# Performance work log

Measured on AMD Instinct MI355X. Metric: run time of the kernel, lower is better.

Reference implementation:

```python
import jax, jax.numpy as jnp
import numpy as np

REPEAT = 3
N, M, APM = 8192, 256, 32   # atoms, molecules, atoms per molecule
F_IN, D = 16, 64            # input atom features, hidden dim (d_e=d_v=d_u)


def _build_graph():
    k1 = np.arange(APM - 1)
    k2 = np.arange(APM - 2)
    pairs = np.concatenate([np.stack([k1, k1 + 1], 1), np.stack([k2, k2 + 2], 1)], 0)  # (61,2)
    base = (np.arange(M) * APM)[:, None, None]
    all_pairs = (pairs[None] + base).reshape(-1, 2)  # (E,2), upper triangular (left<right)
    return all_pairs[:, 0].astype(np.int32), all_pairs[:, 1].astype(np.int32)


def setup_inputs() -> dict:
    key = jax.random.key(0)
    ks = jax.random.split(key, 10)
    left, right = _build_graph()
    E = left.shape[0]  # 15616
    rng = np.random.default_rng(0)
    orders = rng.integers(1, 3, size=E).astype(np.float32)  # bond orders in {1,2}
    adj = np.zeros((N, N), np.float32)
    adj[left, right] = orders
    atom_in_mol = np.zeros((N, M), bool)
    atom_in_mol[np.arange(N), np.arange(N) // APM] = True
    bond_mol = left // APM
    bond_in_mol = np.zeros((E, M), bool)
    bond_in_mol[np.arange(E), bond_mol] = True

    def dense(k, fan_in, fan_out):
        return jax.random.normal(k, (fan_in, fan_out), jnp.float32) / np.sqrt(fan_in)

    return {
        'atoms': jax.random.normal(ks[0], (N, F_IN), jnp.float32),
        'adjacency_map': jnp.asarray(adj),
        'left_idxs': jnp.asarray(left),
        'right_idxs': jnp.asarray(right),
        'atom_in_mol': jnp.asarray(atom_in_mol),
        'bond_in_mol': jnp.asarray(bond_in_mol),
        'W_fe': dense(ks[1], 1, D), 'b_fe': jnp.zeros((D,), jnp.float32),
        'W_fv': dense(ks[2], F_IN, D), 'b_fv': jnp.zeros((D,), jnp.float32),
        'W_fu': dense(ks[3], F_IN, D), 'b_fu': jnp.zeros((D,), jnp.float32),
        'W_pe': dense(ks[4], 4 * D + 1, D), 'b_pe': jnp.zeros((D,), jnp.float32),
        'W_pv': dense(ks[5], 4 * D, D), 'b_pv': jnp.zeros((D,), jnp.float32),
        'W_pu': dense(ks[6], 4 * D, D), 'b_pu': jnp.zeros((D,), jnp.float32),
    }


def _graphnet(atoms, adjacency_map, left_idxs, right_idxs, atom_in_mol, bond_in_mol,
              W_fe, b_fe, W_fv, b_fv, W_fu, b_fu, W_pe, b_pe, W_pv, b_pv, W_pu, b_pu):
    n_atoms = atoms.shape[0]
    n_mols = atom_in_mol.shape[1]
    atom_mol = jnp.argmax(atom_in_mol, axis=1)   # (N,)  one mol per atom
    bond_mol = jnp.argmax(bond_in_mol, axis=1)   # (E,)  one mol per bond

    # f_e / f_v / f_u : initial edge, node, global embeddings
    bond_orders = adjacency_map[left_idxs, right_idxs]                  # (E,)
    h_e = jnp.tanh(bond_orders[:, None] @ W_fe + b_fe)                  # (E,D)
    h_v = jnp.tanh(atoms @ W_fv + b_fv)                                 # (N,D)
    atoms_per_mol = jax.ops.segment_sum(atoms, atom_mol, num_segments=n_mols)
    h_u = jnp.tanh(atoms_per_mol @ W_fu + b_fu)                         # (M,D)
    h_e0, h_v0, h_u0 = h_e, h_v, h_u

    for _ in range(REPEAT):
        # phi_e: per-edge update. TF's global term reduces over the feature
        # axis with keepdims -> a scalar per bond (faithful reproduction).
        h_left = h_v[left_idxs]
        h_right = h_v[right_idxs]
        u_e = jnp.sum(h_u[bond_mol], axis=1, keepdims=True)             # (E,1)
        h_e = jnp.tanh(jnp.concatenate([h_e, h_e0, h_left, h_right, u_e], -1) @ W_pe + b_pe)

        # rho_e_v: masked sum of edge features per incident atom == scatter-add
        h_e_bar_i = (jnp.zeros((n_atoms, h_e.shape[1]), h_e.dtype)
                     .at[left_idxs].add(h_e).at[right_idxs].add(h_e))   # (N,D)
        u_v = h_u[atom_mol]                                             # (N,D)
        h_v = jnp.tanh(jnp.concatenate([h_v, h_v0, h_e_bar_i, u_v], -1) @ W_pv + b_pv)

        # rho_e_u / rho_v_u: masked sums per molecule == segment sums
        h_e_bar = jax.ops.segment_sum(h_e, bond_mol, num_segments=n_mols)
        h_v_bar = jax.ops.segment_sum(h_v, atom_mol, num_segments=n_mols)
        h_u = jnp.tanh(jnp.concatenate([h_u, h_u0, h_e_bar, h_v_bar], -1) @ W_pu + b_pu)

    # default f_r = lambda *x: x[0] -> final edge representations
    return h_e


def reference(atoms, adjacency_map, left_idxs, right_idxs, atom_in_mol, bond_in_mol,
              W_fe, b_fe, W_fv, b_fv, W_fu, b_fu, W_pe, b_pe, W_pv, b_pv, W_pu, b_pu):
    return _graphnet(atoms, adjacency_map, left_idxs, right_idxs, atom_in_mol, bond_in_mol,
                     W_fe, b_fe, W_fv, b_fv, W_fu, b_fu, W_pe, b_pe, W_pv, b_pv, W_pu, b_pu)
```

## Files before the change

kernel.cpp:

```cpp
#include <hip/hip_runtime.h>

#define NATOMS 8192
#define NMOLS  256
#define APM    32
#define EPM    61
#define D      64
#define FIN    16
#define SE     72

typedef __bf16 bf16x8 __attribute__((ext_vector_type(8)));
typedef float  f32x4  __attribute__((ext_vector_type(4)));

#define MFMA_BF16(a, b, c) __builtin_amdgcn_mfma_f32_16x16x32_bf16((a), (b), (c), 0, 0, 0)

__device__ __forceinline__ ushort f2bf(float x) {
    uint u = __float_as_uint(x);
    u += 0x7fffu + ((u >> 16) & 1u);
    return (ushort)(u >> 16);
}
__device__ __forceinline__ float bf2f(ushort h) {
    return __uint_as_float(((uint)h) << 16);
}
__device__ __forceinline__ void split2(float x, ushort& h, ushort& l) {
    ushort hh = f2bf(x);
    h = hh;
    l = f2bf(x - bf2f(hh));
}
__device__ __forceinline__ float fast_tanh(float x) {
    float e = __builtin_amdgcn_exp2f(x * 2.885390081777926f);
    float r = __builtin_amdgcn_rcpf(e + 1.0f);
    return __builtin_fmaf(-2.0f, r, 1.0f);
}

union FragU { ushort u[8]; bf16x8 v; };

__device__ __forceinline__ void mfma3s(const ushort* pH, const ushort* pL, int o,
                                       bf16x8 wH, bf16x8 wL,
                                       f32x4& H, f32x4& La, f32x4& Lb) {
    bf16x8 ah = *(const bf16x8*)(pH + o);
    bf16x8 al = *(const bf16x8*)(pL + o);
    H  = MFMA_BF16(ah, wH, H);
    La = MFMA_BF16(al, wH, La);
    Lb = MFMA_BF16(ah, wL, Lb);
}

__global__ __launch_bounds__(512, 2) void graphnet_kernel(
    const float* __restrict__ atoms,
    const float* __restrict__ adj,
    const int*   __restrict__ left,
    const int*   __restrict__ right,
    const float* __restrict__ Wfe, const float* __restrict__ bfe,
    const float* __restrict__ Wfv, const float* __restrict__ bfv,
    const float* __restrict__ Wfu, const float* __restrict__ bfu,
    const float* __restrict__ Wpe, const float* __restrict__ bpe,
    const float* __restrict__ Wpv, const float* __restrict__ bpv,
    const float* __restrict__ Wpu, const float* __restrict__ bpu,
    float* __restrict__ out)
{
    __shared__ __align__(16) ushort heH[2][64 * SE], heL[2][64 * SE];
    __shared__ __align__(16) ushort hvH[2][APM * SE], hvL[2][APM * SE];
    __shared__ __align__(16) ushort huH[D], huL[D];
    __shared__ float huF[D], hu0F[D];
    __shared__ float atoms_s[APM * FIN];
    __shared__ float apm_s[FIN];
    __shared__ float bo_s[EPM];
    __shared__ float parte[4][D];
    __shared__ float part2[2][D];
    __shared__ float hebar[D];
    __shared__ float phiu_part[8][D];
    __shared__ int   lloc[EPM], rloc[EPM];
    __shared__ int   inc[APM][4];

    const int tid  = threadIdx.x;
    const int lane = tid & 63;
    const int w    = tid >> 6;
    const int nt   = w & 3;
    const int mt2  = w >> 2;
    const int cb   = __builtin_amdgcn_readfirstlane(nt) * 16;
    const int lr   = lane & 15;
    const int kb   = lane >> 4;
    const int m    = blockIdx.x;

    if (tid < EPM) {
        int gl = left [m * EPM + tid];
        int gr = right[m * EPM + tid];
        lloc[tid] = gl - m * APM;
        rloc[tid] = gr - m * APM;
        bo_s[tid] = adj[(size_t)gl * NATOMS + gr];
    }
    if (tid < APM * FIN) atoms_s[tid] = atoms[(size_t)m * (APM * FIN) + tid];

    FragU feH[8], feL[8], fvH[8], fvL[8];
    #pragma unroll
    for (int s = 0; s < 8; ++s) {
        if (s == 2 || s == 3) continue;
        #pragma unroll
        for (int j = 0; j < 8; ++j) {
            split2(Wpe[(s * 32 + kb * 8 + j) * D + cb + lr], feH[s].u[j], feL[s].u[j]);
            split2(Wpv[(s * 32 + kb * 8 + j) * D + cb + lr], fvH[s].u[j], fvL[s].u[j]);
        }
    }
    float wpu_reg[32];
    #pragma unroll
    for (int kk = 0; kk < 32; ++kk)
        wpu_reg[kk] = Wpu[(w * 32 + kk) * D + lane];
    const float bias_e = bpe[cb + lr];
    const float w5_e   = Wpe[4 * D * D + cb + lr];
    const float bias_v = bpv[cb + lr];
    const float bpu_l  = bpu[lane];

    __syncthreads();

    if (tid < APM) {
        int dg = 0;
        for (int e = 0; e < EPM; ++e) {
            if (lloc[e] == tid) inc[tid][dg++] = e;
            if (rloc[e] == tid) inc[tid][dg++] = e;
        }
        for (int j = dg; j < 4; ++j) inc[tid][j] = 63;
    }
    if (tid < FIN) {
        float s = 0.f;
        for (int a = 0; a < APM; ++a) s += atoms_s[a * FIN + tid];
        apm_s[tid] = s;
    }
    #pragma unroll
    for (int i = 0; i < 4; ++i) {
        int idx = tid + 512 * i;
        int a = idx >> 6, c = idx & 63;
        float acc = bfv[c];
        #pragma unroll
        for (int f = 0; f < FIN; ++f) acc += atoms_s[a * FIN + f] * Wfv[f * D + c];
        float t = fast_tanh(acc);
        ushort h, l; split2(t, h, l);
        hvH[0][a * SE + c] = h; hvL[0][a * SE + c] = l;
    }
    #pragma unroll
    for (int i = 0; i < 8; ++i) {
        int idx = tid + 512 * i;
        int e = idx >> 6, c = idx & 63;
        float t = 0.f;
        if (e < EPM) t = fast_tanh(bo_s[e] * Wfe[c] + bfe[c]);
        ushort h, l; split2(t, h, l);
        heH[0][e * SE + c] = h; heL[0][e * SE + c] = l;
        if (e >= EPM) { heH[1][e * SE + c] = 0; heL[1][e * SE + c] = 0; }
    }
    __syncthreads();

    float hu_val;
    {
        float acc = bfu[lane];
        #pragma unroll
        for (int f = 0; f < FIN; ++f) acc += apm_s[f] * Wfu[f * D + lane];
        hu_val = fast_tanh(acc);
        if (w == 7) {
            huF[lane] = hu_val; hu0F[lane] = hu_val;
            split2(hu_val, huH[lane], huL[lane]);
        }
    }

    const int col  = cb + lr;
    const int e0   = mt2 * 16 + lr;
    const int e1   = e0 + 32;
    const int ec1  = (e1 < EPM) ? e1 : EPM - 1;
    const int la0  = lloc[e0],  ra0 = rloc[e0];
    const int la1  = lloc[ec1], ra1 = rloc[ec1];
    const int ofk  = kb * 8;
    const int arow = mt2 * 16 + lr;
    const int ie0 = inc[arow][0], ie1 = inc[arow][1];
    const int ie2 = inc[arow][2], ie3 = inc[arow][3];

    f32x4 cE0 = {bias_e, bias_e, bias_e, bias_e};
    f32x4 cE1 = cE0;
    f32x4 cV  = {bias_v, bias_v, bias_v, bias_v};
    {
        FragU w2h, w2l, w3h, w3l, v2h, v2l, v3h, v3l;
        #pragma unroll
        for (int j = 0; j < 8; ++j) {
            split2(Wpe[(2 * 32 + kb * 8 + j) * D + cb + lr], w2h.u[j], w2l.u[j]);
            split2(Wpe[(3 * 32 + kb * 8 + j) * D + cb + lr], w3h.u[j], w3l.u[j]);
            split2(Wpv[(2 * 32 + kb * 8 + j) * D + cb + lr], v2h.u[j], v2l.u[j]);
            split2(Wpv[(3 * 32 + kb * 8 + j) * D + cb + lr], v3h.u[j], v3l.u[j]);
        }
        f32x4 z0 = {0,0,0,0}, z1 = {0,0,0,0}, z2 = {0,0,0,0},
              z3 = {0,0,0,0}, z4 = {0,0,0,0}, z5 = {0,0,0,0};
        mfma3s(heH[0] + e0*SE,  heL[0] + e0*SE,  ofk,      w2h.v, w2l.v, cE0, z0, z1);
        mfma3s(heH[0] + e1*SE,  heL[0] + e1*SE,  ofk,      w2h.v, w2l.v, cE1, z2, z3);
        mfma3s(heH[0] + e0*SE,  heL[0] + e0*SE,  32 + ofk, w3h.v, w3l.v, cE0, z0, z1);
        mfma3s(heH[0] + e1*SE,  heL[0] + e1*SE,  32 + ofk, w3h.v, w3l.v, cE1, z2, z3);
        mfma3s(hvH[0] + arow*SE, hvL[0] + arow*SE, ofk,      v2h.v, v2l.v, cV, z4, z5);
        mfma3s(hvH[0] + arow*SE, hvL[0] + arow*SE, 32 + ofk, v3h.v, v3l.v, cV, z4, z5);
        cE0 += z0 + z1; cE1 += z2 + z3; cV += z4 + z5;
    }

    int cur = 0;
    for (int it = 0; it < 3; ++it) {
        const ushort* heHc = heH[cur]; const ushort* heLc = heL[cur];
        const ushort* hvHc = hvH[cur]; const ushort* hvLc = hvL[cur];

        f32x4 aH0 = cE0, aL0a = {0,0,0,0}, aL0b = {0,0,0,0};
        f32x4 aH1 = cE1, aL1a = {0,0,0,0}, aL1b = {0,0,0,0};
        mfma3s(heHc + e0*SE,  heLc + e0*SE,  ofk,      feH[0].v, feL[0].v, aH0, aL0a, aL0b);
        mfma3s(heHc + e1*SE,  heLc + e1*SE,  ofk,      feH[0].v, feL[0].v, aH1, aL1a, aL1b);
        mfma3s(heHc + e0*SE,  heLc + e0*SE,  32 + ofk, feH[1].v, feL[1].v, aH0, aL0a, aL0b);
        mfma3s(heHc + e1*SE,  heLc + e1*SE,  32 + ofk, feH[1].v, feL[1].v, aH1, aL1a, aL1b);
        mfma3s(hvHc + la0*SE, hvLc + la0*SE, ofk,      feH[4].v, feL[4].v, aH0, aL0a, aL0b);
        mfma3s(hvHc + la1*SE, hvLc + la1*SE, ofk,      feH[4].v, feL[4].v, aH1, aL1a, aL1b);
        mfma3s(hvHc + la0*SE, hvLc + la0*SE, 32 + ofk, feH[5].v, feL[5].v, aH0, aL0a, aL0b);
        mfma3s(hvHc + la1*SE, hvLc + la1*SE, 32 + ofk, feH[5].v, feL[5].v, aH1, aL1a, aL1b);
        mfma3s(hvHc + ra0*SE, hvLc + ra0*SE, ofk,      feH[6].v, feL[6].v, aH0, aL0a, aL0b);
        mfma3s(hvHc + ra1*SE, hvLc + ra1*SE, ofk,      feH[6].v, feL[6].v, aH1, aL1a, aL1b);
        mfma3s(hvHc + ra0*SE, hvLc + ra0*SE, 32 + ofk, feH[7].v, feL[7].v, aH0, aL0a, aL0b);
        mfma3s(hvHc + ra1*SE, hvLc + ra1*SE, 32 + ofk, feH[7].v, feL[7].v, aH1, aL1a, aL1b);

        if (it > 0) {
            float t = bpu_l;
            #pragma unroll
            for (int w8 = 0; w8 < 8; ++w8) t += phiu_part[w8][lane];
            hu_val = fast_tanh(t);
            if (w == 7) {
                huF[lane] = hu_val;
                split2(hu_val, huH[lane], huL[lane]);
            }
        }
        float uev = hu_val;
        #pragma unroll
        for (int off = 32; off; off >>= 1) uev += __shfl_xor(uev, off, 64);

        float out0[4], out1[4]; float ps0 = 0.f, ps1 = 0.f;
        #pragma unroll
        for (int r = 0; r < 4; ++r) {
            float t0 = fast_tanh(aH0[r] + aL0a[r] + aL0b[r] + uev * w5_e);
            float t1 = fast_tanh(aH1[r] + aL1a[r] + aL1b[r] + uev * w5_e);
            out0[r] = t0; out1[r] = t1;
            ps0 += t0;
            if (32 + mt2 * 16 + kb * 4 + r < EPM) ps1 += t1;
        }

        if (it == 2) {
            #pragma unroll
            for (int r = 0; r < 4; ++r) {
                int g0 = mt2 * 16 + kb * 4 + r;
                out[((size_t)(m * EPM + g0)) * D + col] = out0[r];
                int g1 = g0 + 32;
                if (g1 < EPM) out[((size_t)(m * EPM + g1)) * D + col] = out1[r];
            }
            return;
        }

        ps0 += __shfl_xor(ps0, 16, 64); ps0 += __shfl_xor(ps0, 32, 64);
        ps1 += __shfl_xor(ps1, 16, 64); ps1 += __shfl_xor(ps1, 32, 64);

        const int nxt = cur ^ 1;
        #pragma unroll
        for (int r = 0; r < 4; ++r) {
            int g0 = mt2 * 16 + kb * 4 + r;
            split2(out0[r], heH[nxt][g0 * SE + col], heL[nxt][g0 * SE + col]);
            int g1 = g0 + 32;
            if (g1 < EPM)
                split2(out1[r], heH[nxt][g1 * SE + col], heL[nxt][g1 * SE + col]);
        }
        if (kb == 0) { parte[mt2][col] = ps0; parte[2 + mt2][col] = ps1; }
        __syncthreads();

        const ushort* heHn = heH[nxt]; const ushort* heLn = heL[nxt];

        f32x4 vH = cV, vLa = {0,0,0,0}, vLb = {0,0,0,0};
        mfma3s(hvHc + arow*SE, hvLc + arow*SE, ofk,      fvH[0].v, fvL[0].v, vH, vLa, vLb);
        mfma3s(hvHc + arow*SE, hvLc + arow*SE, 32 + ofk, fvH[1].v, fvL[1].v, vH, vLa, vLb);
        mfma3s(heHn + ie0*SE, heLn + ie0*SE, ofk,      fvH[4].v, fvL[4].v, vH, vLa, vLb);
        mfma3s(heHn + ie0*SE, heLn + ie0*SE, 32 + ofk, fvH[5].v, fvL[5].v, vH, vLa, vLb);
        mfma3s(heHn + ie1*SE, heLn + ie1*SE, ofk,      fvH[4].v, fvL[4].v, vH, vLa, vLb);
        mfma3s(heHn + ie1*SE, heLn + ie1*SE, 32 + ofk, fvH[5].v, fvL[5].v, vH, vLa, vLb);
        mfma3s(heHn + ie2*SE, heLn + ie2*SE, ofk,      fvH[4].v, fvL[4].v, vH, vLa, vLb);
        mfma3s(heHn + ie2*SE, heLn + ie2*SE, 32 + ofk, fvH[5].v, fvL[5].v, vH, vLa, vLb);
        mfma3s(heHn + ie3*SE, heLn + ie3*SE, ofk,      fvH[4].v, fvL[4].v, vH, vLa, vLb);
        mfma3s(heHn + ie3*SE, heLn + ie3*SE, 32 + ofk, fvH[5].v, fvL[5].v, vH, vLa, vLb);
        mfma3s(huH, huL, ofk,      fvH[6].v, fvL[6].v, vH, vLa, vLb);
        mfma3s(huH, huL, 32 + ofk, fvH[7].v, fvL[7].v, vH, vLa, vLb);

        if (tid < D)
            hebar[tid] = parte[0][tid] + parte[1][tid] + parte[2][tid] + parte[3][tid];

        float outv2[4]; float ps2 = 0.f;
        #pragma unroll
        for (int r = 0; r < 4; ++r) {
            float t = fast_tanh(vH[r] + vLa[r] + vLb[r]);
            outv2[r] = t; ps2 += t;
        }
        ps2 += __shfl_xor(ps2, 16, 64); ps2 += __shfl_xor(ps2, 32, 64);
        #pragma unroll
        for (int r = 0; r < 4; ++r) {
            int g = mt2 * 16 + kb * 4 + r;
            split2(outv2[r], hvH[nxt][g * SE + col], hvL[nxt][g * SE + col]);
        }
        if (kb == 0) part2[mt2][col] = ps2;
        __syncthreads();

        {
            const int b  = w >> 1;
            const int k0 = (w & 1) * 32;
            float s = 0.f;
            #pragma unroll
            for (int kk = 0; kk < 32; ++kk) {
                int k = k0 + kk;
                float x = (b == 0) ? huF[k] : (b == 1) ? hu0F[k]
                        : (b == 2) ? hebar[k] : (part2[0][k] + part2[1][k]);
                s += x * wpu_reg[kk];
            }
            phiu_part[w][lane] = s;
        }
        __syncthreads();
        cur = nxt;
    }
}

extern "C" void kernel_launch(void* const* d_in, const int* in_sizes, int n_in,
                              void* d_out, int out_size, void* d_ws, size_t ws_size,
                              hipStream_t stream) {
    const float* atoms = (const float*)d_in[0];
    const float* adj   = (const float*)d_in[1];
    const int*   left  = (const int*)  d_in[2];
    const int*   right = (const int*)  d_in[3];
    const float* Wfe = (const float*)d_in[6];
    const float* bfe = (const float*)d_in[7];
    const float* Wfv = (const float*)d_in[8];
    const float* bfv = (const float*)d_in[9];
    const float* Wfu = (const float*)d_in[10];
    const float* bfu = (const float*)d_in[11];
    const float* Wpe = (const float*)d_in[12];
    const float* bpe = (const float*)d_in[13];
    const float* Wpv = (const float*)d_in[14];
    const float* bpv = (const float*)d_in[15];
    const float* Wpu = (const float*)d_in[16];
    const float* bpu = (const float*)d_in[17];

    graphnet_kernel<<<dim3(NMOLS), dim3(512), 0, stream>>>(
        atoms, adj, left, right,
        Wfe, bfe, Wfv, bfv, Wfu, bfu,
        Wpe, bpe, Wpv, bpv, Wpu, bpu,
        (float*)d_out);
}
```

Baseline: 37.11 us.

## Double block to 1024 threads and stage split weight fragments in LDS

Launches 1024 threads per molecule, so each wave handles one 16-row edge tile instead of two, and only half the waves compute the vertex update. Pre-split bf16 hi/lo weight fragments for the edge and vertex MLPs are now built cooperatively once and stored in a 96KB LDS buffer, replacing per-wave register copies. This is meant to cut register pressure and shorten each wave's serial MFMA chain. The cost is roughly 96KB of extra shared memory per block, which limits residency to one block per CU, plus an LDS load for every weight fragment. The atom and bond-order staging buffers are also dropped in favour of direct global reads.

```diff
diff --git a/kernel.cpp b/kernel.cpp
--- a/kernel.cpp
+++ b/kernel.cpp
@@ -43,8 +43,19 @@
     La = MFMA_BF16(al, wH, La);
     Lb = MFMA_BF16(ah, wL, Lb);
 }
-
-__global__ __launch_bounds__(512, 2) void graphnet_kernel(
+__device__ __forceinline__ void mfma3w(const ushort* pH, const ushort* pL, int o,
+                                       const ushort* wHp, const ushort* wLp,
+                                       f32x4& H, f32x4& La, f32x4& Lb) {
+    bf16x8 ah = *(const bf16x8*)(pH + o);
+    bf16x8 al = *(const bf16x8*)(pL + o);
+    bf16x8 wH = *(const bf16x8*)wHp;
+    bf16x8 wL = *(const bf16x8*)wLp;
+    H  = MFMA_BF16(ah, wH, H);
+    La = MFMA_BF16(al, wH, La);
+    Lb = MFMA_BF16(ah, wL, Lb);
+}
+
+__global__ __launch_bounds__(1024) void graphnet_kernel(
     const float* __restrict__ atoms,
     const float* __restrict__ adj,
     const int*   __restrict__ left,
@@ -57,13 +68,12 @@
     const float* __restrict__ Wpu, const float* __restrict__ bpu,
     float* __restrict__ out)
 {
+    __shared__ __align__(16) ushort wlds[49152];
     __shared__ __align__(16) ushort heH[2][64 * SE], heL[2][64 * SE];
     __shared__ __align__(16) ushort hvH[2][APM * SE], hvL[2][APM * SE];
     __shared__ __align__(16) ushort huH[D], huL[D];
     __shared__ float huF[D], hu0F[D];
-    __shared__ float atoms_s[APM * FIN];
     __shared__ float apm_s[FIN];
-    __shared__ float bo_s[EPM];
     __shared__ float parte[4][D];
     __shared__ float part2[2][D];
     __shared__ float hebar[D];
@@ -75,35 +85,41 @@
     const int lane = tid & 63;
     const int w    = tid >> 6;
     const int nt   = w & 3;
-    const int mt2  = w >> 2;
+    const int mt4  = w >> 2;
     const int cb   = __builtin_amdgcn_readfirstlane(nt) * 16;
     const int lr   = lane & 15;
     const int kb   = lane >> 4;
     const int m    = blockIdx.x;
 
+#define WFR(mat, si, hl) ((const ushort*)wlds + \
+    ((((mat)*6+(si))*4+nt)*2+(hl))*512 + (lane << 3))
+
     if (tid < EPM) {
-        int gl = left [m * EPM + tid];
-        int gr = right[m * EPM + tid];
-        lloc[tid] = gl - m * APM;
-        rloc[tid] = gr - m * APM;
-        bo_s[tid] = adj[(size_t)gl * NATOMS + gr];
-    }
-    if (tid < APM * FIN) atoms_s[tid] = atoms[(size_t)m * (APM * FIN) + tid];
-
-    FragU feH[8], feL[8], fvH[8], fvL[8];
+        lloc[tid] = left [m * EPM + tid] - m * APM;
+        rloc[tid] = right[m * EPM + tid] - m * APM;
+    }
+
     #pragma unroll
-    for (int s = 0; s < 8; ++s) {
-        if (s == 2 || s == 3) continue;
-        #pragma unroll
-        for (int j = 0; j < 8; ++j) {
-            split2(Wpe[(s * 32 + kb * 8 + j) * D + cb + lr], feH[s].u[j], feL[s].u[j]);
-            split2(Wpv[(s * 32 + kb * 8 + j) * D + cb + lr], fvH[s].u[j], fvL[s].u[j]);
-        }
+    for (int p = 0; p < 3; ++p) {
+        int pid = w * 3 + p;
+        int mat = pid / 24;
+        int rem = pid - mat * 24;
+        int si  = rem >> 2;
+        int ntp = rem & 3;
+        int s   = si + ((si >= 2) ? 2 : 0);
+        const float* W = mat ? Wpv : Wpe;
+        FragU fh, fl;
+        #pragma unroll
+        for (int j = 0; j < 8; ++j)
+            split2(W[(s * 32 + kb * 8 + j) * D + ntp * 16 + lr], fh.u[j], fl.u[j]);
+        int base = (((mat * 6 + si) * 4 + ntp) * 2) * 512 + (lane << 3);
+        *(bf16x8*)(wlds + base)       = fh.v;
+        *(bf16x8*)(wlds + base + 512) = fl.v;
     }
     float wpu_reg[32];
     #pragma unroll
     for (int kk = 0; kk < 32; ++kk)
-        wpu_reg[kk] = Wpu[(w * 32 + kk) * D + lane];
+        wpu_reg[kk] = Wpu[((w & 7) * 32 + kk) * D + lane];
     const float bias_e = bpe[cb + lr];
     const float w5_e   = Wpe[4 * D * D + cb + lr];
     const float bias_v = bpv[cb + lr];
@@ -121,26 +137,32 @@
     }
     if (tid < FIN) {
         float s = 0.f;
-        for (int a = 0; a < APM; ++a) s += atoms_s[a * FIN + tid];
+        for (int a = 0; a < APM; ++a) s += atoms[(m * APM + a) * FIN + tid];
         apm_s[tid] = s;
     }
     #pragma unroll
-    for (int i = 0; i < 4; ++i) {
-        int idx = tid + 512 * i;
+    for (int i = 0; i < 2; ++i) {
+        int idx = tid + 1024 * i;
         int a = idx >> 6, c = idx & 63;
         float acc = bfv[c];
         #pragma unroll
-        for (int f = 0; f < FIN; ++f) acc += atoms_s[a * FIN + f] * Wfv[f * D + c];
+        for (int f = 0; f < FIN; ++f)
+            acc += atoms[(m * APM + a) * FIN + f] * Wfv[f * D + c];
         float t = fast_tanh(acc);
         ushort h, l; split2(t, h, l);
         hvH[0][a * SE + c] = h; hvL[0][a * SE + c] = l;
     }
     #pragma unroll
-    for (int i = 0; i < 8; ++i) {
-        int idx = tid + 512 * i;
+    for (int i = 0; i < 4; ++i) {
+        int idx = tid + 1024 * i;
         int e = idx >> 6, c = idx & 63;
         float t = 0.f;
-        if (e < EPM) t = fast_tanh(bo_s[e] * Wfe[c] + bfe[c]);
+        if (e < EPM) {
+            int gl = left [m * EPM + e];
+            int gr = right[m * EPM + e];
+            float bo = adj[(size_t)gl * NATOMS + gr];
+            t = fast_tanh(bo * Wfe[c] + bfe[c]);
+        }
         ushort h, l; split2(t, h, l);
         heH[0][e * SE + c] = h; heL[0][e * SE + c] = l;
         if (e >= EPM) { heH[1][e * SE + c] = 0; heL[1][e * SE + c] = 0; }
@@ -153,26 +175,23 @@
         #pragma unroll
         for (int f = 0; f < FIN; ++f) acc += apm_s[f] * Wfu[f * D + lane];
         hu_val = fast_tanh(acc);
-        if (w == 7) {
+        if (w == 15) {
             huF[lane] = hu_val; hu0F[lane] = hu_val;
             split2(hu_val, huH[lane], huL[lane]);
         }
     }
 
-    const int col  = cb + lr;
-    const int e0   = mt2 * 16 + lr;
-    const int e1   = e0 + 32;
-    const int ec1  = (e1 < EPM) ? e1 : EPM - 1;
-    const int la0  = lloc[e0],  ra0 = rloc[e0];
-    const int la1  = lloc[ec1], ra1 = rloc[ec1];
-    const int ofk  = kb * 8;
-    const int arow = mt2 * 16 + lr;
+    const int col   = cb + lr;
+    const int erow  = mt4 * 16 + lr;
+    const int ec    = (erow < EPM) ? erow : EPM - 1;
+    const int la0   = lloc[ec], ra0 = rloc[ec];
+    const int ofk   = kb * 8;
+    const int arow  = (mt4 & 1) * 16 + lr;
     const int ie0 = inc[arow][0], ie1 = inc[arow][1];
     const int ie2 = inc[arow][2], ie3 = inc[arow][3];
 
-    f32x4 cE0 = {bias_e, bias_e, bias_e, bias_e};
-    f32x4 cE1 = cE0;
-    f32x4 cV  = {bias_v, bias_v, bias_v, bias_v};
+    f32x4 cE = {bias_e, bias_e, bias_e, bias_e};
+    f32x4 cV = {bias_v, bias_v, bias_v, bias_v};
     {
         FragU w2h, w2l, w3h, w3l, v2h, v2l, v3h, v3l;
         #pragma unroll
@@ -182,15 +201,12 @@
             split2(Wpv[(2 * 32 + kb * 8 + j) * D + cb + lr], v2h.u[j], v2l.u[j]);
             split2(Wpv[(3 * 32 + kb * 8 + j) * D + cb + lr], v3h.u[j], v3l.u[j]);
         }
-        f32x4 z0 = {0,0,0,0}, z1 = {0,0,0,0}, z2 = {0,0,0,0},
-              z3 = {0,0,0,0}, z4 = {0,0,0,0}, z5 = {0,0,0,0};
-        mfma3s(heH[0] + e0*SE,  heL[0] + e0*SE,  ofk,      w2h.v, w2l.v, cE0, z0, z1);
-        mfma3s(heH[0] + e1*SE,  heL[0] + e1*SE,  ofk,      w2h.v, w2l.v, cE1, z2, z3);
-        mfma3s(heH[0] + e0*SE,  heL[0] + e0*SE,  32 + ofk, w3h.v, w3l.v, cE0, z0, z1);
-        mfma3s(heH[0] + e1*SE,  heL[0] + e1*SE,  32 + ofk, w3h.v, w3l.v, cE1, z2, z3);
+        f32x4 z0 = {0,0,0,0}, z1 = {0,0,0,0}, z4 = {0,0,0,0}, z5 = {0,0,0,0};
+        mfma3s(heH[0] + erow*SE, heL[0] + erow*SE, ofk,      w2h.v, w2l.v, cE, z0, z1);
+        mfma3s(heH[0] + erow*SE, heL[0] + erow*SE, 32 + ofk, w3h.v, w3l.v, cE, z0, z1);
         mfma3s(hvH[0] + arow*SE, hvL[0] + arow*SE, ofk,      v2h.v, v2l.v, cV, z4, z5);
         mfma3s(hvH[0] + arow*SE, hvL[0] + arow*SE, 32 + ofk, v3h.v, v3l.v, cV, z4, z5);
-        cE0 += z0 + z1; cE1 += z2 + z3; cV += z4 + z5;
+        cE += z0 + z1; cV += z4 + z5;
     }
 
     int cur = 0;
@@ -198,27 +214,20 @@
         const ushort* heHc = heH[cur]; const ushort* heLc = heL[cur];
         const ushort* hvHc = hvH[cur]; const ushort* hvLc = hvL[cur];
 
-        f32x4 aH0 = cE0, aL0a = {0,0,0,0}, aL0b = {0,0,0,0};
-        f32x4 aH1 = cE1, aL1a = {0,0,0,0}, aL1b = {0,0,0,0};
-        mfma3s(heHc + e0*SE,  heLc + e0*SE,  ofk,      feH[0].v, feL[0].v, aH0, aL0a, aL0b);
-        mfma3s(heHc + e1*SE,  heLc + e1*SE,  ofk,      feH[0].v, feL[0].v, aH1, aL1a, aL1b);
-        mfma3s(heHc + e0*SE,  heLc + e0*SE,  32 + ofk, feH[1].v, feL[1].v, aH0, aL0a, aL0b);
-        mfma3s(heHc + e1*SE,  heLc + e1*SE,  32 + ofk, feH[1].v, feL[1].v, aH1, aL1a, aL1b);
-        mfma3s(hvHc + la0*SE, hvLc + la0*SE, ofk,      feH[4].v, feL[4].v, aH0, aL0a, aL0b);
-        mfma3s(hvHc + la1*SE, hvLc + la1*SE, ofk,      feH[4].v, feL[4].v, aH1, aL1a, aL1b);
-        mfma3s(hvHc + la0*SE, hvLc + la0*SE, 32 + ofk, feH[5].v, feL[5].v, aH0, aL0a, aL0b);
-        mfma3s(hvHc + la1*SE, hvLc + la1*SE, 32 + ofk, feH[5].v, feL[5].v, aH1, aL1a, aL1b);
-        mfma3s(hvHc + ra0*SE, hvLc + ra0*SE, ofk,      feH[6].v, feL[6].v, aH0, aL0a, aL0b);
-        mfma3s(hvHc + ra1*SE, hvLc + ra1*SE, ofk,      feH[6].v, feL[6].v, aH1, aL1a, aL1b);
-        mfma3s(hvHc + ra0*SE, hvLc + ra0*SE, 32 + ofk, feH[7].v, feL[7].v, aH0, aL0a, aL0b);
-        mfma3s(hvHc + ra1*SE, hvLc + ra1*SE, 32 + ofk, feH[7].v, feL[7].v, aH1, aL1a, aL1b);
+        f32x4 aH = cE, aLa = {0,0,0,0}, aLb = {0,0,0,0};
+        mfma3w(heHc + erow*SE, heLc + erow*SE, ofk,      WFR(0,0,0), WFR(0,0,1), aH, aLa, aLb);
+        mfma3w(heHc + erow*SE, heLc + erow*SE, 32 + ofk, WFR(0,1,0), WFR(0,1,1), aH, aLa, aLb);
+        mfma3w(hvHc + la0*SE,  hvLc + la0*SE,  ofk,      WFR(0,2,0), WFR(0,2,1), aH, aLa, aLb);
+        mfma3w(hvHc + la0*SE,  hvLc + la0*SE,  32 + ofk, WFR(0,3,0), WFR(0,3,1), aH, aLa, aLb);
+        mfma3w(hvHc + ra0*SE,  hvLc + ra0*SE,  ofk,      WFR(0,4,0), WFR(0,4,1), aH, aLa, aLb);
+        mfma3w(hvHc + ra0*SE,  hvLc + ra0*SE,  32 + ofk, WFR(0,5,0), WFR(0,5,1), aH, aLa, aLb);
 
         if (it > 0) {
             float t = bpu_l;
             #pragma unroll
             for (int w8 = 0; w8 < 8; ++w8) t += phiu_part[w8][lane];
             hu_val = fast_tanh(t);
-            if (w == 7) {
+            if (w == 15) {
                 huF[lane] = hu_val;
                 split2(hu_val, huH[lane], huL[lane]);
             }
@@ -227,77 +236,71 @@
         #pragma unroll
         for (int off = 32; off; off >>= 1) uev += __shfl_xor(uev, off, 64);
 
-        float out0[4], out1[4]; float ps0 = 0.f, ps1 = 0.f;
+        float out0[4]; float ps0 = 0.f;
         #pragma unroll
         for (int r = 0; r < 4; ++r) {
-            float t0 = fast_tanh(aH0[r] + aL0a[r] + aL0b[r] + uev * w5_e);
-            float t1 = fast_tanh(aH1[r] + aL1a[r] + aL1b[r] + uev * w5_e);
-            out0[r] = t0; out1[r] = t1;
-            ps0 += t0;
-            if (32 + mt2 * 16 + kb * 4 + r < EPM) ps1 += t1;
+            float t0 = fast_tanh(aH[r] + aLa[r] + aLb[r] + uev * w5_e);
+            out0[r] = t0;
+            if (mt4 * 16 + kb * 4 + r < EPM) ps0 += t0;
         }
 
         if (it == 2) {
             #pragma unroll
             for (int r = 0; r < 4; ++r) {
-                int g0 = mt2 * 16 + kb * 4 + r;
-                out[((size_t)(m * EPM + g0)) * D + col] = out0[r];
-                int g1 = g0 + 32;
-                if (g1 < EPM) out[((size_t)(m * EPM + g1)) * D + col] = out1[r];
+                int g = mt4 * 16 + kb * 4 + r;
+                if (g < EPM) out[((size_t)(m * EPM + g)) * D + col] = out0[r];
             }
             return;
         }
 
         ps0 += __shfl_xor(ps0, 16, 64); ps0 += __shfl_xor(ps0, 32, 64);
-        ps1 += __shfl_xor(ps1, 16, 64); ps1 += __shfl_xor(ps1, 32, 64);
 
         const int nxt = cur ^ 1;
         #pragma unroll
         for (int r = 0; r < 4; ++r) {
-            int g0 = mt2 * 16 + kb * 4 + r;
-            split2(out0[r], heH[nxt][g0 * SE + col], heL[nxt][g0 * SE + col]);
-            int g1 = g0 + 32;
-            if (g1 < EPM)
-                split2(out1[r], heH[nxt][g1 * SE + col], heL[nxt][g1 * SE + col]);
-        }
-        if (kb == 0) { parte[mt2][col] = ps0; parte[2 + mt2][col] = ps1; }
+            int g = mt4 * 16 + kb * 4 + r;
+            if (g < EPM)
+                split2(out0[r], heH[nxt][g * SE + col], heL[nxt][g * SE + col]);
+        }
+        if (kb == 0) parte[mt4][col] = ps0;
         __syncthreads();
 
         const ushort* heHn = heH[nxt]; const ushort* heLn = heL[nxt];
 
-        f32x4 vH = cV, vLa = {0,0,0,0}, vLb = {0,0,0,0};
-        mfma3s(hvHc + arow*SE, hvLc + arow*SE, ofk,      fvH[0].v, fvL[0].v, vH, vLa, vLb);
-        mfma3s(hvHc + arow*SE, hvLc + arow*SE, 32 + ofk, fvH[1].v, fvL[1].v, vH, vLa, vLb);
-        mfma3s(heHn + ie0*SE, heLn + ie0*SE, ofk,      fvH[4].v, fvL[4].v, vH, vLa, vLb);
-        mfma3s(heHn + ie0*SE, heLn + ie0*SE, 32 + ofk, fvH[5].v, fvL[5].v, vH, vLa, vLb);
-        mfma3s(heHn + ie1*SE, heLn + ie1*SE, ofk,      fvH[4].v, fvL[4].v, vH, vLa, vLb);
-        mfma3s(heHn + ie1*SE, heLn + ie1*SE, 32 + ofk, fvH[5].v, fvL[5].v, vH, vLa, vLb);
-        mfma3s(heHn + ie2*SE, heLn + ie2*SE, ofk,      fvH[4].v, fvL[4].v, vH, vLa, vLb);
-        mfma3s(heHn + ie2*SE, heLn + ie2*SE, 32 + ofk, fvH[5].v, fvL[5].v, vH, vLa, vLb);
-        mfma3s(heHn + ie3*SE, heLn + ie3*SE, ofk,      fvH[4].v, fvL[4].v, vH, vLa, vLb);
-        mfma3s(heHn + ie3*SE, heLn + ie3*SE, 32 + ofk, fvH[5].v, fvL[5].v, vH, vLa, vLb);
-        mfma3s(huH, huL, ofk,      fvH[6].v, fvL[6].v, vH, vLa, vLb);
-        mfma3s(huH, huL, 32 + ofk, fvH[7].v, fvL[7].v, vH, vLa, vLb);
-
-        if (tid < D)
-            hebar[tid] = parte[0][tid] + parte[1][tid] + parte[2][tid] + parte[3][tid];
-
-        float outv2[4]; float ps2 = 0.f;
-        #pragma unroll
-        for (int r = 0; r < 4; ++r) {
-            float t = fast_tanh(vH[r] + vLa[r] + vLb[r]);
-            outv2[r] = t; ps2 += t;
-        }
-        ps2 += __shfl_xor(ps2, 16, 64); ps2 += __shfl_xor(ps2, 32, 64);
-        #pragma unroll
-        for (int r = 0; r < 4; ++r) {
-            int g = mt2 * 16 + kb * 4 + r;
-            split2(outv2[r], hvH[nxt][g * SE + col], hvL[nxt][g * SE + col]);
-        }
-        if (kb == 0) part2[mt2][col] = ps2;
+        if (mt4 < 2) {
+            f32x4 vH = cV, vLa = {0,0,0,0}, vLb = {0,0,0,0};
+            mfma3w(hvHc + arow*SE, hvLc + arow*SE, ofk,      WFR(1,0,0), WFR(1,0,1), vH, vLa, vLb);
+            mfma3w(hvHc + arow*SE, hvLc + arow*SE, 32 + ofk, WFR(1,1,0), WFR(1,1,1), vH, vLa, vLb);
+            mfma3w(heHn + ie0*SE, heLn + ie0*SE, ofk,      WFR(1,2,0), WFR(1,2,1), vH, vLa, vLb);
+            mfma3w(heHn + ie0*SE, heLn + ie0*SE, 32 + ofk, WFR(1,3,0), WFR(1,3,1), vH, vLa, vLb);
+            mfma3w(heHn + ie1*SE, heLn + ie1*SE, ofk,      WFR(1,2,0), WFR(1,2,1), vH, vLa, vLb);
+            mfma3w(heHn + ie1*SE, heLn + ie1*SE, 32 + ofk, WFR(1,3,0), WFR(1,3,1), vH, vLa, vLb);
+            mfma3w(heHn + ie2*SE, heLn + ie2*SE, ofk,      WFR(1,2,0), WFR(1,2,1), vH, vLa, vLb);
+            mfma3w(heHn + ie2*SE, heLn + ie2*SE, 32 + ofk, WFR(1,3,0), WFR(1,3,1), vH, vLa, vLb);
+            mfma3w(heHn + ie3*SE, heLn + ie3*SE, ofk,      WFR(1,2,0), WFR(1,2,1), vH, vLa, vLb);
+            mfma3w(heHn + ie3*SE, heLn + ie3*SE, 32 + ofk, WFR(1,3,0), WFR(1,3,1), vH, vLa, vLb);
+            mfma3w(huH, huL, ofk,      WFR(1,4,0), WFR(1,4,1), vH, vLa, vLb);
+            mfma3w(huH, huL, 32 + ofk, WFR(1,5,0), WFR(1,5,1), vH, vLa, vLb);
+
+            float outv2[4]; float ps2 = 0.f;
+            #pragma unroll
+            for (int r = 0; r < 4; ++r) {
+                float t = fast_tanh(vH[r] + vLa[r] + vLb[r]);
+                outv2[r] = t; ps2 += t;
+            }
+            ps2 += __shfl_xor(ps2, 16, 64); ps2 += __shfl_xor(ps2, 32, 64);
+            #pragma unroll
+            for (int r = 0; r < 4; ++r) {
+                int g = (mt4 & 1) * 16 + kb * 4 + r;
+                split2(outv2[r], hvH[nxt][g * SE + col], hvL[nxt][g * SE + col]);
+            }
+            if (kb == 0) part2[mt4][col] = ps2;
+        } else if (w == 8) {
+            hebar[lane] = parte[0][lane] + parte[1][lane] + parte[2][lane] + parte[3][lane];
+        }
         __syncthreads();
 
-        {
+        if (w < 8) {
             const int b  = w >> 1;
             const int k0 = (w & 1) * 32;
             float s = 0.f;
@@ -335,7 +338,7 @@
     const float* Wpu = (const float*)d_in[16];
     const float* bpu = (const float*)d_in[17];
 
-    graphnet_kernel<<<dim3(NMOLS), dim3(512), 0, stream>>>(
+    graphnet_kernel<<<dim3(NMOLS), dim3(1024), 0, stream>>>(
         atoms, adj, left, right,
         Wfe, bfe, Wfv, bfv, Wfu, bfu,
         Wpe, bpe, Wpv, bpv, Wpu, bpu,
```

Result: slower. 43.15 us (+16.3%).
